# Kernel optimization log

Measured on AMD Instinct MI355X. Metric: run time of the kernel, lower is better.

## Reference

```python
import jax, jax.numpy as jnp
import numpy as np

Z_DIM = 2  # state dimension is hard-coded (fc1: Linear(2, H), fc3: Linear(H, 2))


def _mlp(z, W1, b1, W2, b2, W3, b3):
    # torch.nn.Linear: y = x @ W.T + b
    h = jax.nn.elu(z @ W1.T + b1)
    h = jax.nn.elu(h @ W2.T + b2)
    return h @ W3.T + b3


def setup_inputs() -> dict:
    key = jax.random.key(0)
    ks = jax.random.split(key, 8)
    B, H = 1_000_000, 64
    s_in = 1.0 / np.sqrt(Z_DIM)
    s_h = 1.0 / np.sqrt(H)
    u = lambda k, shp, s: jax.random.uniform(k, shp, jnp.float32, -s, s)
    return {
        "t": jax.random.normal(ks[0], (1,), jnp.float32),
        "z_and_logp": jax.random.normal(ks[1], (B, Z_DIM + 1), jnp.float32),
        "W1": u(ks[2], (H, Z_DIM), s_in),
        "b1": u(ks[3], (H,), s_in),
        "W2": u(ks[4], (H, H), s_h),
        "b2": u(ks[5], (H,), s_h),
        "W3": u(ks[6], (Z_DIM, H), s_h),
        "b3": u(ks[7], (Z_DIM,), s_h),
    }


def reference(t, z_and_logp, W1, b1, W2, b2, W3, b3):
    # t is an unused time argument (ODE solver interface).
    z = z_and_logp[:, :Z_DIM]  # [B, 2]; logp column is not used in forward
    f = lambda x: _mlp(x, W1, b1, W2, b2, W3, b3)

    # Exact Jacobian trace via forward-mode JVPs with unit tangents (Z_DIM=2,
    # so this small fixed loop mirrors the per-dim autograd loop in torch).
    dz_dt = None
    trace = jnp.zeros(z.shape[0], dtype=z.dtype)
    for i in range(Z_DIM):
        e = jnp.zeros_like(z).at[:, i].set(1.0)
        out, jz = jax.jvp(f, (z,), (e,))
        if dz_dt is None:
            dz_dt = out
        trace = trace + jz[:, i]

    dlogp_dt = -trace[:, None]  # [B, 1]
    return jnp.concatenate([dz_dt, dlogp_dt], axis=1)  # [B, 3]
```

## Files before the change

### kernel.cpp

```cpp
#include <hip/hip_runtime.h>
#include <hip/hip_bf16.h>


typedef short bf16x8 __attribute__((ext_vector_type(8)));
typedef float f32x4  __attribute__((ext_vector_type(4)));
typedef int   i32x4  __attribute__((ext_vector_type(4)));

static __device__ __forceinline__ short f2bf(float x) {
    __hip_bfloat16 b = __float2bfloat16(x);
    return __builtin_bit_cast(short, b);
}

static __device__ __forceinline__ int cvt_pk_bf16(float lo, float hi) {
    int r;
    asm("v_cvt_pk_bf16_f32 %0, %1, %2" : "=v"(r) : "v"(lo), "v"(hi));
    return r;
}

__global__ __launch_bounds__(256) __attribute__((amdgpu_waves_per_eu(3, 3)))
void odefunc_mfma(const float* __restrict__ zin,
                  const float* __restrict__ W1, const float* __restrict__ b1,
                  const float* __restrict__ W2, const float* __restrict__ b2,
                  const float* __restrict__ W3, const float* __restrict__ b3,
                  float* __restrict__ out, int B, int ntiles)
{
    __shared__ f32x4 sC[96];

    const int lane = threadIdx.x & 63;
    const int quad = lane >> 4;
    const int col  = lane & 15;

    if (threadIdx.x < 64) {
        int i = threadIdx.x;
        float* s = (float*)sC;
        s[i]       = W1[2*i];
        s[64 + i]  = W1[2*i + 1];
        s[128 + i] = b1[i];
        s[192 + i] = b2[i];
        s[256 + i] = W3[i];
        s[320 + i] = W3[64 + i];
    }

    const int wid    = blockIdx.x * (blockDim.x >> 6) + (threadIdx.x >> 6);
    const int nwaves = gridDim.x * (blockDim.x >> 6);

    bf16x8 aW2[4][2], aG[4][2];
#pragma unroll
    for (int mt = 0; mt < 4; ++mt) {
        const int k = mt * 16 + col;
        const float ck = W3[k], dk = W3[64 + k];
#pragma unroll
        for (int jt = 0; jt < 2; ++jt) {
            const float* p = W2 + k * 64 + jt * 32 + quad * 8;
#pragma unroll
            for (int jj = 0; jj < 8; ++jj) {
                int j = jt * 32 + quad * 8 + jj;
                float w2 = p[jj];
                aW2[mt][jt][jj] = f2bf(w2);
                aG[mt][jt][jj]  = f2bf(w2 * fmaf(ck, W1[2*j], dk * W1[2*j+1]));
            }
        }
    }

    const float b30 = b3[0], b31 = b3[1];
    const f32x4 zero4 = {0.f, 0.f, 0.f, 0.f};

    __syncthreads();

    const int lload = lane < 48 ? lane : 47;
    int t = wid;
    float zv = 0.f;
    if (t < ntiles) zv = zin[t * 48 + lload];

    int cofs = 0;
    for (; t < ntiles; t += nwaves) {
        asm volatile("" : "+v"(cofs));

        int tn = t + nwaves;
        int tc = tn < ntiles ? tn : t;
        float zvn = zin[tc * 48 + lload];

        float z0 = __shfl(zv, 3 * col);
        float z1 = __shfl(zv, 3 * col + 1);

        bf16x8 Bh[2], Bex[2];
#pragma unroll
        for (int jt = 0; jt < 2; ++jt) {
            int j4 = cofs + jt * 8 + quad * 2;
            f32x4 w0a = sC[j4],      w0b = sC[j4 + 1];
            f32x4 w1a = sC[j4 + 16], w1b = sC[j4 + 17];
            f32x4 bba = sC[j4 + 32], bbb = sC[j4 + 33];
            float h[8], ex[8];
#pragma unroll
            for (int jj = 0; jj < 8; ++jj) {
                float w0 = (jj < 4) ? w0a[jj & 3] : w0b[jj & 3];
                float w1 = (jj < 4) ? w1a[jj & 3] : w1b[jj & 3];
                float bb = (jj < 4) ? bba[jj & 3] : bbb[jj & 3];
                float a  = fmaf(w0, z0, fmaf(w1, z1, bb));
                float e  = __expf(fminf(a, 0.f));
                ex[jj] = e;
                h[jj]  = fmaxf(a, 0.f) + (e - 1.f);
            }
            i32x4 ph, pe;
#pragma unroll
            for (int d = 0; d < 4; ++d) {
                ph[d] = cvt_pk_bf16(h[2*d],  h[2*d+1]);
                pe[d] = cvt_pk_bf16(ex[2*d], ex[2*d+1]);
            }
            Bh[jt]  = __builtin_bit_cast(bf16x8, ph);
            Bex[jt] = __builtin_bit_cast(bf16x8, pe);
        }

        f32x4 accH[4], accT[4];
#pragma unroll
        for (int mt = 0; mt < 4; ++mt) {
            accH[mt] = __builtin_amdgcn_mfma_f32_16x16x32_bf16(aW2[mt][0], Bh[0], zero4, 0, 0, 0);
            accH[mt] = __builtin_amdgcn_mfma_f32_16x16x32_bf16(aW2[mt][1], Bh[1], accH[mt], 0, 0, 0);
            accT[mt] = __builtin_amdgcn_mfma_f32_16x16x32_bf16(aG[mt][0], Bex[0], zero4, 0, 0, 0);
            accT[mt] = __builtin_amdgcn_mfma_f32_16x16x32_bf16(aG[mt][1], Bex[1], accT[mt], 0, 0, 0);
        }

        float o0 = 0.f, o1 = 0.f, trc = 0.f;
#pragma unroll
        for (int mt = 0; mt < 4; ++mt) {
            int k4 = cofs + 48 + mt * 4 + quad;
            f32x4 b2v = sC[k4];
            f32x4 w30 = sC[k4 + 16];
            f32x4 w31 = sC[k4 + 32];
#pragma unroll
            for (int i = 0; i < 4; ++i) {
                float a2  = accH[mt][i] + b2v[i];
                float e2  = __expf(fminf(a2, 0.f));
                float hh  = fmaxf(a2, 0.f) + (e2 - 1.f);
                o0  = fmaf(w30[i], hh, o0);
                o1  = fmaf(w31[i], hh, o1);
                trc = fmaf(e2, accT[mt][i], trc);
            }
        }

        o0  += __shfl_xor(o0, 16);  o0  += __shfl_xor(o0, 32);
        o1  += __shfl_xor(o1, 16);  o1  += __shfl_xor(o1, 32);
        trc += __shfl_xor(trc, 16); trc += __shfl_xor(trc, 32);

        int row = t * 16 + col;
        if (lane < 16 && row < B) {
            out[3 * row + 0] = o0 + b30;
            out[3 * row + 1] = o1 + b31;
            out[3 * row + 2] = -trc;
        }

        zv = zvn;
    }
}

extern "C" void kernel_launch(void* const* d_in, const int* in_sizes, int n_in,
                              void* d_out, int out_size, void* d_ws, size_t ws_size,
                              hipStream_t stream) {
    const float* zin = (const float*)d_in[1];
    const float* W1  = (const float*)d_in[2];
    const float* b1  = (const float*)d_in[3];
    const float* W2  = (const float*)d_in[4];
    const float* b2  = (const float*)d_in[5];
    const float* W3  = (const float*)d_in[6];
    const float* b3  = (const float*)d_in[7];
    float* out = (float*)d_out;

    int B = in_sizes[1] / 3;
    int ntiles = (B + 15) / 16;
    int grid = 1536;
    odefunc_mfma<<<grid, 256, 0, stream>>>(zin, W1, b1, W2, b2, W3, b3,
                                           out, B, ntiles);
}
```

Baseline: 128.9 us.

## Pack elementwise ELU math into paired f32 ops and raise occupancy

Rewrites the per-element ELU work in both layers as 2-wide float vector ops so the compiler can emit packed FMA/min/max/add instructions, and computes exp through the exp2 builtin with an explicit log2(e) scale. The b2 bias now goes in as the initial MFMA accumulator rather than being added afterwards, and the W3/b2 shared-memory loads are hoisted ahead of the MFMAs. Waves per EU rises from 3 to 4 and the grid from 1536 to 2048 blocks, aiming to hide more latency. The main risk is register pressure under the tighter occupancy target, which could cause spills. Summing the packed partials in a different order can also shift floating-point rounding slightly.

```diff
diff --git a/kernel.cpp b/kernel.cpp
--- a/kernel.cpp
+++ b/kernel.cpp
@@ -4,7 +4,11 @@
 
 typedef short bf16x8 __attribute__((ext_vector_type(8)));
 typedef float f32x4  __attribute__((ext_vector_type(4)));
+typedef float f32x2  __attribute__((ext_vector_type(2)));
 typedef int   i32x4  __attribute__((ext_vector_type(4)));
+
+#define LO2(v) __builtin_shufflevector(v, v, 0, 1)
+#define HI2(v) __builtin_shufflevector(v, v, 2, 3)
 
 static __device__ __forceinline__ short f2bf(float x) {
     __hip_bfloat16 b = __float2bfloat16(x);
@@ -17,7 +21,7 @@
     return r;
 }
 
-__global__ __launch_bounds__(256) __attribute__((amdgpu_waves_per_eu(3, 3)))
+__global__ __launch_bounds__(256) __attribute__((amdgpu_waves_per_eu(4, 4)))
 void odefunc_mfma(const float* __restrict__ zin,
                   const float* __restrict__ W1, const float* __restrict__ b1,
                   const float* __restrict__ W2, const float* __restrict__ b2,
@@ -64,6 +68,9 @@
 
     const float b30 = b3[0], b31 = b3[1];
     const f32x4 zero4 = {0.f, 0.f, 0.f, 0.f};
+    const f32x2 zerop = {0.f, 0.f};
+    const f32x2 m1p   = {-1.f, -1.f};
+    const f32x2 l2e   = {1.442695040888963f, 1.442695040888963f};
 
     __syncthreads();
 
@@ -82,6 +89,7 @@
 
         float z0 = __shfl(zv, 3 * col);
         float z1 = __shfl(zv, 3 * col + 1);
+        const f32x2 z0p = {z0, z0}, z1p = {z1, z1};
 
         bf16x8 Bh[2], Bex[2];
 #pragma unroll
@@ -90,53 +98,67 @@
             f32x4 w0a = sC[j4],      w0b = sC[j4 + 1];
             f32x4 w1a = sC[j4 + 16], w1b = sC[j4 + 17];
             f32x4 bba = sC[j4 + 32], bbb = sC[j4 + 33];
-            float h[8], ex[8];
-#pragma unroll
-            for (int jj = 0; jj < 8; ++jj) {
-                float w0 = (jj < 4) ? w0a[jj & 3] : w0b[jj & 3];
-                float w1 = (jj < 4) ? w1a[jj & 3] : w1b[jj & 3];
-                float bb = (jj < 4) ? bba[jj & 3] : bbb[jj & 3];
-                float a  = fmaf(w0, z0, fmaf(w1, z1, bb));
-                float e  = __expf(fminf(a, 0.f));
-                ex[jj] = e;
-                h[jj]  = fmaxf(a, 0.f) + (e - 1.f);
-            }
             i32x4 ph, pe;
 #pragma unroll
-            for (int d = 0; d < 4; ++d) {
-                ph[d] = cvt_pk_bf16(h[2*d],  h[2*d+1]);
-                pe[d] = cvt_pk_bf16(ex[2*d], ex[2*d+1]);
+            for (int p = 0; p < 4; ++p) {
+                f32x2 w0p = (p == 0) ? LO2(w0a) : (p == 1) ? HI2(w0a)
+                           : (p == 2) ? LO2(w0b) : HI2(w0b);
+                f32x2 w1p = (p == 0) ? LO2(w1a) : (p == 1) ? HI2(w1a)
+                           : (p == 2) ? LO2(w1b) : HI2(w1b);
+                f32x2 bbp = (p == 0) ? LO2(bba) : (p == 1) ? HI2(bba)
+                           : (p == 2) ? LO2(bbb) : HI2(bbb);
+                f32x2 a  = __builtin_elementwise_fma(w0p, z0p,
+                           __builtin_elementwise_fma(w1p, z1p, bbp));
+                f32x2 am = __builtin_elementwise_min(a, zerop);
+                f32x2 tt = am * l2e;
+                f32x2 e  = { __builtin_amdgcn_exp2f(tt[0]),
+                             __builtin_amdgcn_exp2f(tt[1]) };
+                f32x2 rl = __builtin_elementwise_max(a, zerop);
+                f32x2 h  = rl + (e + m1p);
+                ph[p] = cvt_pk_bf16(h[0], h[1]);
+                pe[p] = cvt_pk_bf16(e[0], e[1]);
             }
             Bh[jt]  = __builtin_bit_cast(bf16x8, ph);
             Bex[jt] = __builtin_bit_cast(bf16x8, pe);
         }
 
         f32x4 accH[4], accT[4];
+        f32x4 w30q[4], w31q[4];
 #pragma unroll
         for (int mt = 0; mt < 4; ++mt) {
-            accH[mt] = __builtin_amdgcn_mfma_f32_16x16x32_bf16(aW2[mt][0], Bh[0], zero4, 0, 0, 0);
+            int k4 = cofs + 48 + mt * 4 + quad;
+            f32x4 b2v = sC[k4];
+            w30q[mt] = sC[k4 + 16];
+            w31q[mt] = sC[k4 + 32];
+            accH[mt] = __builtin_amdgcn_mfma_f32_16x16x32_bf16(aW2[mt][0], Bh[0], b2v, 0, 0, 0);
             accH[mt] = __builtin_amdgcn_mfma_f32_16x16x32_bf16(aW2[mt][1], Bh[1], accH[mt], 0, 0, 0);
             accT[mt] = __builtin_amdgcn_mfma_f32_16x16x32_bf16(aG[mt][0], Bex[0], zero4, 0, 0, 0);
             accT[mt] = __builtin_amdgcn_mfma_f32_16x16x32_bf16(aG[mt][1], Bex[1], accT[mt], 0, 0, 0);
         }
 
-        float o0 = 0.f, o1 = 0.f, trc = 0.f;
+        f32x2 o0p = zerop, o1p = zerop, trcp = zerop;
 #pragma unroll
         for (int mt = 0; mt < 4; ++mt) {
-            int k4 = cofs + 48 + mt * 4 + quad;
-            f32x4 b2v = sC[k4];
-            f32x4 w30 = sC[k4 + 16];
-            f32x4 w31 = sC[k4 + 32];
 #pragma unroll
-            for (int i = 0; i < 4; ++i) {
-                float a2  = accH[mt][i] + b2v[i];
-                float e2  = __expf(fminf(a2, 0.f));
-                float hh  = fmaxf(a2, 0.f) + (e2 - 1.f);
-                o0  = fmaf(w30[i], hh, o0);
-                o1  = fmaf(w31[i], hh, o1);
-                trc = fmaf(e2, accT[mt][i], trc);
+            for (int half = 0; half < 2; ++half) {
+                f32x2 a2  = half ? HI2(accH[mt]) : LO2(accH[mt]);
+                f32x2 at  = half ? HI2(accT[mt]) : LO2(accT[mt]);
+                f32x2 w30 = half ? HI2(w30q[mt]) : LO2(w30q[mt]);
+                f32x2 w31 = half ? HI2(w31q[mt]) : LO2(w31q[mt]);
+                f32x2 am = __builtin_elementwise_min(a2, zerop);
+                f32x2 tt = am * l2e;
+                f32x2 e  = { __builtin_amdgcn_exp2f(tt[0]),
+                             __builtin_amdgcn_exp2f(tt[1]) };
+                f32x2 rl = __builtin_elementwise_max(a2, zerop);
+                f32x2 hh = rl + (e + m1p);
+                o0p  = __builtin_elementwise_fma(w30, hh, o0p);
+                o1p  = __builtin_elementwise_fma(w31, hh, o1p);
+                trcp = __builtin_elementwise_fma(e, at, trcp);
             }
         }
+        float o0 = o0p[0] + o0p[1];
+        float o1 = o1p[0] + o1p[1];
+        float trc = trcp[0] + trcp[1];
 
         o0  += __shfl_xor(o0, 16);  o0  += __shfl_xor(o0, 32);
         o1  += __shfl_xor(o1, 16);  o1  += __shfl_xor(o1, 32);
@@ -167,7 +189,7 @@
 
     int B = in_sizes[1] / 3;
     int ntiles = (B + 15) / 16;
-    int grid = 1536;
+    int grid = 2048;
     odefunc_mfma<<<grid, 256, 0, stream>>>(zin, W1, b1, W2, b2, W3, b3,
                                            out, B, ntiles);
 }
```

New measurement: 131.0 us. About the same (+1.6%).
